# Kernel optimization log

Measured on AMD Instinct MI355X. Metric: run time of the kernel, lower is better.

## Reference

```python
import jax, jax.numpy as jnp
import numpy as np

N, D = 256, 512
DIST_W, ANGLE_W = 1.0, 2.0
EPS_PD = 1e-6    # F.pairwise_distance eps (added to the difference)
EPS_COS = 1e-8   # F.cosine_similarity eps (denominator floor)
CLAMP = 1e-7     # acos clamp margin


def _smooth_l1(x):
    # F.smooth_l1_loss with beta=1.0, elementwise (reduction handled by caller)
    ax = jnp.abs(x)
    return jnp.where(ax < 1.0, 0.5 * ax * ax, ax - 0.5)


def _pairwise_dist(E):
    # Faithful to the looped version: dist[i,j] = ||e_i - e_j + eps|| for i<j,
    # mirrored to the lower triangle, zero diagonal.
    diff = E[:, None, :] - E[None, :, :] + EPS_PD          # [n, n, d]
    d = jnp.sqrt(jnp.sum(diff * diff, axis=-1))            # [n, n]
    upper = jnp.triu(d, k=1)
    return upper + upper.T


def _angles(E):
    # ang[j, i, k] = angle at vertex j between (e_i - e_j) and (e_k - e_j)
    Dv = E[None, :, :] - E[:, None, :]                     # Dv[j, a] = e_a - e_j
    norms = jnp.sqrt(jnp.sum(Dv * Dv, axis=-1))            # [n, n]
    dots = jnp.einsum('jad,jbd->jab', Dv, Dv)              # [n, n, n]
    denom = jnp.maximum(norms[:, :, None] * norms[:, None, :], EPS_COS)
    cos = jnp.clip(dots / denom, -1.0 + CLAMP, 1.0 - CLAMP)
    return jnp.arccos(cos)


def setup_inputs() -> dict:
    key = jax.random.key(0)
    k1, k2 = jax.random.split(key)
    return {
        'student_embeddings': jax.random.normal(k1, (N, D), dtype=jnp.float32),
        'teacher_embeddings': jax.random.normal(k2, (N, D), dtype=jnp.float32),
    }


def reference(student_embeddings, teacher_embeddings):
    # distance-wise loss: smooth_l1 mean over the full n x n matrix
    ds = _pairwise_dist(student_embeddings)
    dt = _pairwise_dist(teacher_embeddings)
    distance_loss = jnp.mean(_smooth_l1(ds - dt))

    # angle-wise loss: mean over triplets i<j<k (vertex at j)
    n = student_embeddings.shape[0]
    ang_s = _angles(student_embeddings)
    ang_t = _angles(teacher_embeddings)
    idx = jnp.arange(n)
    # mask[j, i, k] = (i < j) & (j < k)
    mask = (idx[None, :, None] < idx[:, None, None]) & (idx[:, None, None] < idx[None, None, :])
    count = n * (n - 1) * (n - 2) // 6
    angle_loss = jnp.sum(_smooth_l1(ang_s - ang_t) * mask) / count

    total_loss = DIST_W * distance_loss + ANGLE_W * angle_loss
    return (total_loss, distance_loss, angle_loss)
```

## Files before the change

### kernel.cpp

```cpp
#include <hip/hip_runtime.h>
#include <math.h>

#define N 256
#define D 512
#define KT 64
#define LDSPAD 68
#define SPLIT 4

__device__ __forceinline__ float smooth_l1(float x) {
    float ax = fabsf(x);
    return ax < 1.f ? 0.5f * ax * ax : ax - 0.5f;
}

__global__ __launch_bounds__(256) void gram_kernel(const float* __restrict__ Es,
                                                   const float* __restrict__ Et,
                                                   float* __restrict__ Gs,
                                                   float* __restrict__ Gt,
                                                   float* __restrict__ acc) {
    const float* E = blockIdx.z ? Et : Es;
    float* G = blockIdx.z ? Gt : Gs;
    __shared__ __align__(16) float As[16 * LDSPAD];
    __shared__ __align__(16) float Bs[16 * LDSPAD];
    const int tx = threadIdx.x, ty = threadIdx.y;
    const int t = ty * 16 + tx;
    if (blockIdx.x == 0 && blockIdx.y == 0 && blockIdx.z == 0 && t == 0) {
        acc[0] = 0.f;
        acc[1] = 0.f;
    }
    const int lr = t >> 4;
    const int lc = (t & 15) * 4;
    const int rowA = blockIdx.y * 16 + lr;
    const int rowB = blockIdx.x * 16 + lr;
    float sum = 0.f;
    for (int k0 = 0; k0 < D; k0 += KT) {
        float4 a4 = *(const float4*)&E[rowA * D + k0 + lc];
        float4 b4 = *(const float4*)&E[rowB * D + k0 + lc];
        *(float4*)&As[lr * LDSPAD + lc] = a4;
        *(float4*)&Bs[lr * LDSPAD + lc] = b4;
        __syncthreads();
        const float4* Ar = (const float4*)&As[ty * LDSPAD];
        const float4* Br = (const float4*)&Bs[tx * LDSPAD];
#pragma unroll
        for (int kk = 0; kk < KT / 4; ++kk) {
            float4 a = Ar[kk], b = Br[kk];
            sum += a.x * b.x + a.y * b.y + a.z * b.z + a.w * b.w;
        }
        __syncthreads();
    }
    G[(blockIdx.y * 16 + ty) * N + blockIdx.x * 16 + tx] = sum;
}

__global__ __launch_bounds__(256) void angle_dist_kernel(const float* __restrict__ Gs,
                                                         const float* __restrict__ Gt,
                                                         float* __restrict__ acc) {
    const int j = blockIdx.x + 1;
    const int tid = threadIdx.x;
    __shared__ float cs[N], ct[N], rns[N], rnt[N];
    __shared__ float2 red[256];
    const float Gsjj = Gs[j * N + j];
    const float Gtjj = Gt[j * N + j];

    float distp = 0.f;
    {
        const int a = tid;
        float cja = Gs[a * N + j];
        float cjb = Gt[a * N + j];
        cs[a] = cja;
        ct[a] = cjb;
        float n2s = Gs[a * N + a] - 2.f * cja + Gsjj;
        float n2t = Gt[a * N + a] - 2.f * cjb + Gtjj;
        float rs = (a == j) ? 0.f : rsqrtf(n2s);
        float rt = (a == j) ? 0.f : rsqrtf(n2t);
        rns[a] = rs;
        rnt[a] = rt;
        if (blockIdx.y == 0 && a < j) {
            distp = smooth_l1(n2s * rs - n2t * rt);
        }
    }
    __syncthreads();

    const int nk = 255 - j;
    const int npairs = j * nk;
    const float inv_nk = 1.0f / (float)nk;
    const float lo = -0.99999994f;
    const float hi = 0.99999994f;

    float anglep = 0.f;
    for (int p = blockIdx.y * 256 + tid; p < npairs; p += 256 * SPLIT) {
        int i = (int)((float)p * inv_nk);
        int rem = p - i * nk;
        if (rem < 0) { --i; rem += nk; }
        else if (rem >= nk) { ++i; rem -= nk; }
        const int k = j + 1 + rem;
        float dots = Gs[i * N + k] - cs[i] - cs[k] + Gsjj;
        float dott = Gt[i * N + k] - ct[i] - ct[k] + Gtjj;
        float coss = dots * (rns[i] * rns[k]);
        float cost = dott * (rnt[i] * rnt[k]);
        coss = fminf(fmaxf(coss, lo), hi);
        cost = fminf(fmaxf(cost, lo), hi);
        anglep += smooth_l1(acosf(coss) - acosf(cost));
    }

    red[tid] = make_float2(distp, anglep);
    __syncthreads();
    for (int s = 128; s > 0; s >>= 1) {
        if (tid < s) {
            red[tid].x += red[tid + s].x;
            red[tid].y += red[tid + s].y;
        }
        __syncthreads();
    }
    if (tid == 0) {
        atomicAdd(&acc[1], red[0].y);
        if (blockIdx.y == 0) atomicAdd(&acc[0], red[0].x);
    }
}

__global__ void finalize_kernel(const float* __restrict__ acc,
                                float* __restrict__ out) {
    float dl = 2.f * acc[0] / (float)(N * N);
    float al = acc[1] / (float)(N * (N - 1) * (N - 2) / 6);
    out[0] = 1.0f * dl + 2.0f * al;
    out[1] = dl;
    out[2] = al;
}

extern "C" void kernel_launch(void* const* d_in, const int* in_sizes, int n_in,
                              void* d_out, int out_size, void* d_ws, size_t ws_size,
                              hipStream_t stream) {
    const float* Es = (const float*)d_in[0];
    const float* Et = (const float*)d_in[1];
    float* out = (float*)d_out;
    float* ws = (float*)d_ws;

    float* acc = ws;
    float* Gs  = ws + 64;
    float* Gt  = Gs + N * N;

    gram_kernel<<<dim3(16, 16, 2), dim3(16, 16), 0, stream>>>(Es, Et, Gs, Gt, acc);
    angle_dist_kernel<<<dim3(N - 1, SPLIT), 256, 0, stream>>>(Gs, Gt, acc);
    finalize_kernel<<<1, 1, 0, stream>>>(acc, out);
}
```

Baseline: 87.51 us.

## Use symmetric 32x32 gram tiles, pack LDS vectors, fuse finalize via last-block counter

The gram kernel now computes only upper-triangular 32x32 tiles with a 2x2 register block per thread and writes each result to both mirrored positions, roughly halving the Gram FLOPs and raising reuse per LDS load. The angle kernel packs the centered-dot and reciprocal-norm values into float2 LDS arrays so each lookup is a single load. The finalize kernel is removed: the last block, found through an atomic counter, computes the outputs, which saves one launch at the cost of a threadfence and an extra atomic per block.

```diff
diff --git a/kernel.cpp b/kernel.cpp
--- a/kernel.cpp
+++ b/kernel.cpp
@@ -3,13 +3,18 @@
 
 #define N 256
 #define D 512
-#define KT 64
-#define LDSPAD 68
 #define SPLIT 4
+#define NTILE 8
+#define NUPPER (NTILE * (NTILE + 1) / 2)
+#define KROW 68
 
 __device__ __forceinline__ float smooth_l1(float x) {
     float ax = fabsf(x);
     return ax < 1.f ? 0.5f * ax * ax : ax - 0.5f;
+}
+
+__device__ __forceinline__ float dot4(float4 a, float4 b) {
+    return a.x * b.x + a.y * b.y + a.z * b.z + a.w * b.w;
 }
 
 __global__ __launch_bounds__(256) void gram_kernel(const float* __restrict__ Es,
@@ -19,43 +24,62 @@
                                                    float* __restrict__ acc) {
     const float* E = blockIdx.z ? Et : Es;
     float* G = blockIdx.z ? Gt : Gs;
-    __shared__ __align__(16) float As[16 * LDSPAD];
-    __shared__ __align__(16) float Bs[16 * LDSPAD];
-    const int tx = threadIdx.x, ty = threadIdx.y;
-    const int t = ty * 16 + tx;
-    if (blockIdx.x == 0 && blockIdx.y == 0 && blockIdx.z == 0 && t == 0) {
+    const int t = threadIdx.x;
+
+    if (blockIdx.x == 0 && blockIdx.z == 0 && t == 0) {
         acc[0] = 0.f;
         acc[1] = 0.f;
+        *(unsigned int*)&acc[2] = 0u;
     }
-    const int lr = t >> 4;
-    const int lc = (t & 15) * 4;
-    const int rowA = blockIdx.y * 16 + lr;
-    const int rowB = blockIdx.x * 16 + lr;
-    float sum = 0.f;
-    for (int k0 = 0; k0 < D; k0 += KT) {
-        float4 a4 = *(const float4*)&E[rowA * D + k0 + lc];
-        float4 b4 = *(const float4*)&E[rowB * D + k0 + lc];
-        *(float4*)&As[lr * LDSPAD + lc] = a4;
-        *(float4*)&Bs[lr * LDSPAD + lc] = b4;
+
+    int bi = 0, rem = blockIdx.x;
+    while (rem >= NTILE - bi) { rem -= NTILE - bi; ++bi; }
+    const int bj = bi + rem;
+
+    __shared__ __align__(16) float As[32 * KROW];
+    __shared__ __align__(16) float Bs[32 * KROW];
+
+    const int tx = t & 15, ty = t >> 4;
+    float s00 = 0.f, s01 = 0.f, s10 = 0.f, s11 = 0.f;
+
+    for (int k0 = 0; k0 < D; k0 += 64) {
+#pragma unroll
+        for (int s = t; s < 512; s += 256) {
+            const int r = s >> 4, c = (s & 15) * 4;
+            *(float4*)&As[r * KROW + c] = *(const float4*)&E[(bi * 32 + r) * D + k0 + c];
+            *(float4*)&Bs[r * KROW + c] = *(const float4*)&E[(bj * 32 + r) * D + k0 + c];
+        }
         __syncthreads();
-        const float4* Ar = (const float4*)&As[ty * LDSPAD];
-        const float4* Br = (const float4*)&Bs[tx * LDSPAD];
+        const float4* A0 = (const float4*)&As[ty * KROW];
+        const float4* A1 = (const float4*)&As[(ty + 16) * KROW];
+        const float4* B0 = (const float4*)&Bs[tx * KROW];
+        const float4* B1 = (const float4*)&Bs[(tx + 16) * KROW];
 #pragma unroll
-        for (int kk = 0; kk < KT / 4; ++kk) {
-            float4 a = Ar[kk], b = Br[kk];
-            sum += a.x * b.x + a.y * b.y + a.z * b.z + a.w * b.w;
+        for (int kk = 0; kk < 16; ++kk) {
+            float4 a0 = A0[kk], a1 = A1[kk], b0 = B0[kk], b1 = B1[kk];
+            s00 += dot4(a0, b0);
+            s01 += dot4(a0, b1);
+            s10 += dot4(a1, b0);
+            s11 += dot4(a1, b1);
         }
         __syncthreads();
     }
-    G[(blockIdx.y * 16 + ty) * N + blockIdx.x * 16 + tx] = sum;
+
+    const int r0 = bi * 32 + ty, r1 = r0 + 16;
+    const int c0 = bj * 32 + tx, c1 = c0 + 16;
+    G[r0 * N + c0] = s00;  G[c0 * N + r0] = s00;
+    G[r0 * N + c1] = s01;  G[c1 * N + r0] = s01;
+    G[r1 * N + c0] = s10;  G[c0 * N + r1] = s10;
+    G[r1 * N + c1] = s11;  G[c1 * N + r1] = s11;
 }
 
 __global__ __launch_bounds__(256) void angle_dist_kernel(const float* __restrict__ Gs,
                                                          const float* __restrict__ Gt,
-                                                         float* __restrict__ acc) {
+                                                         float* __restrict__ acc,
+                                                         float* __restrict__ out) {
     const int j = blockIdx.x + 1;
     const int tid = threadIdx.x;
-    __shared__ float cs[N], ct[N], rns[N], rnt[N];
+    __shared__ float2 sv[N], tv[N];
     __shared__ float2 red[256];
     const float Gsjj = Gs[j * N + j];
     const float Gtjj = Gt[j * N + j];
@@ -65,17 +89,14 @@
         const int a = tid;
         float cja = Gs[a * N + j];
         float cjb = Gt[a * N + j];
-        cs[a] = cja;
-        ct[a] = cjb;
         float n2s = Gs[a * N + a] - 2.f * cja + Gsjj;
         float n2t = Gt[a * N + a] - 2.f * cjb + Gtjj;
         float rs = (a == j) ? 0.f : rsqrtf(n2s);
         float rt = (a == j) ? 0.f : rsqrtf(n2t);
-        rns[a] = rs;
-        rnt[a] = rt;
-        if (blockIdx.y == 0 && a < j) {
+        sv[a] = make_float2(cja, rs);
+        tv[a] = make_float2(cjb, rt);
+        if (blockIdx.y == 0 && a < j)
             distp = smooth_l1(n2s * rs - n2t * rt);
-        }
     }
     __syncthreads();
 
@@ -92,12 +113,12 @@
         if (rem < 0) { --i; rem += nk; }
         else if (rem >= nk) { ++i; rem -= nk; }
         const int k = j + 1 + rem;
-        float dots = Gs[i * N + k] - cs[i] - cs[k] + Gsjj;
-        float dott = Gt[i * N + k] - ct[i] - ct[k] + Gtjj;
-        float coss = dots * (rns[i] * rns[k]);
-        float cost = dott * (rnt[i] * rnt[k]);
-        coss = fminf(fmaxf(coss, lo), hi);
-        cost = fminf(fmaxf(cost, lo), hi);
+        float2 si = sv[i], sk = sv[k];
+        float2 ti = tv[i], tk = tv[k];
+        float dots = Gs[i * N + k] - si.x - sk.x + Gsjj;
+        float dott = Gt[i * N + k] - ti.x - tk.x + Gtjj;
+        float coss = fminf(fmaxf(dots * (si.y * sk.y), lo), hi);
+        float cost = fminf(fmaxf(dott * (ti.y * tk.y), lo), hi);
         anglep += smooth_l1(acosf(coss) - acosf(cost));
     }
 
@@ -113,16 +134,18 @@
     if (tid == 0) {
         atomicAdd(&acc[1], red[0].y);
         if (blockIdx.y == 0) atomicAdd(&acc[0], red[0].x);
+        __threadfence();
+        unsigned int old = atomicAdd((unsigned int*)&acc[2], 1u);
+        if (old == (N - 1) * SPLIT - 1) {
+            float ds = atomicAdd(&acc[0], 0.f);
+            float as = atomicAdd(&acc[1], 0.f);
+            float dl = 2.f * ds / (float)(N * N);
+            float al = as / (float)(N * (N - 1) * (N - 2) / 6);
+            out[0] = 1.0f * dl + 2.0f * al;
+            out[1] = dl;
+            out[2] = al;
+        }
     }
-}
-
-__global__ void finalize_kernel(const float* __restrict__ acc,
-                                float* __restrict__ out) {
-    float dl = 2.f * acc[0] / (float)(N * N);
-    float al = acc[1] / (float)(N * (N - 1) * (N - 2) / 6);
-    out[0] = 1.0f * dl + 2.0f * al;
-    out[1] = dl;
-    out[2] = al;
 }
 
 extern "C" void kernel_launch(void* const* d_in, const int* in_sizes, int n_in,
@@ -137,7 +160,6 @@
     float* Gs  = ws + 64;
     float* Gt  = Gs + N * N;
 
-    gram_kernel<<<dim3(16, 16, 2), dim3(16, 16), 0, stream>>>(Es, Et, Gs, Gt, acc);
-    angle_dist_kernel<<<dim3(N - 1, SPLIT), 256, 0, stream>>>(Gs, Gt, acc);
-    finalize_kernel<<<1, 1, 0, stream>>>(acc, out);
+    gram_kernel<<<dim3(NUPPER, 1, 2), 256, 0, stream>>>(Es, Et, Gs, Gt, acc);
+    angle_dist_kernel<<<dim3(N - 1, SPLIT), 256, 0, stream>>>(Gs, Gt, acc, out);
 }
```

After: 107.1 us. 22.4% more time.
